# Optimization experiments

Hardware: AMD Instinct MI355X
Metric: run time of the kernel (lower is better)

## Reference

```python
import jax, jax.numpy as jnp
import numpy as np

FP4_MAX = 6.0  # largest E2M1 magnitude


def _round_fp4(y):
    # Round to nearest value on the FP4 E2M1 grid {0, +-0.5, 1, 1.5, 2, 3, 4, 6}.
    a = jnp.abs(y)
    e = jnp.floor(jnp.log2(jnp.maximum(a, 1.0)))  # 0 for a<2, 1 for [2,4), 2 for >=4
    step = jnp.exp2(e - 1.0)                      # grid spacing: 0.5, 1, 2
    q = jnp.clip(jnp.round(a / step) * step, 0.0, FP4_MAX)
    return jnp.sign(y) * q


def _ste_round_fp4(y):
    # straight-through estimator: identity gradient through the rounding
    return y + jax.lax.stop_gradient(_round_fp4(y) - y)


def _mxfp4_quant(x, group_size, eps=None):
    # Groupwise MXFP4 quant-dequant along the last axis.
    lead, d = x.shape[:-1], x.shape[-1]
    g = d // group_size
    xg = x.reshape(lead + (g, group_size))
    amax = jnp.max(jnp.abs(xg), axis=-1, keepdims=True)
    # shared exponent per MX spec: floor(log2(amax)) - emax_elem (emax_elem = 2 for FP4)
    exps = jnp.where(amax > 0.0,
                     jnp.floor(jnp.log2(jnp.maximum(amax, 1e-30))) - 2.0,
                     0.0)
    scale = jnp.exp2(exps)
    if eps is not None:
        # learnable (adversarially perturbed) per-group scale epsilon
        scale = scale * (1.0 + eps[..., None])
    y = xg / scale
    xq = _ste_round_fp4(y) * scale
    return xq.reshape(x.shape), jnp.squeeze(exps, -1)


def setup_inputs() -> dict:
    key = jax.random.key(0)
    ks = jax.random.split(key, 4)
    B, S, DIN, DOUT, GS = 4, 2048, 4096, 4096, 32
    x = jax.random.normal(ks[0], (B, S, DIN), jnp.float32)
    weight_fp = jax.random.normal(ks[1], (DOUT, DIN), jnp.float32) * 0.02  # frozen FP weight
    bias = jax.random.normal(ks[2], (DOUT,), jnp.float32) * 0.01
    eps = jnp.zeros((DOUT, DIN // GS), jnp.float32)  # learnable weight-quant epsilon
    adversarial_delta = jax.random.normal(ks[3], (DOUT, DIN // GS), jnp.float32) * 0.01
    return {"x": x, "adversarial_delta": adversarial_delta,
            "weight_fp": weight_fp, "bias": bias, "eps": eps}


def reference(x, adversarial_delta, weight_fp, bias, eps):
    GS = 32
    # dynamic activation MXFP4 quantization
    x_q, act_exps = _mxfp4_quant(x, GS)
    # weight MXFP4 quantization with learnable + adversarial epsilon
    eps_eff = eps + adversarial_delta
    w_q, w_exps = _mxfp4_quant(weight_fp, GS, eps_eff)
    # F.linear(x_q, w_q, bias)
    out = jnp.einsum('bsi,oi->bso', x_q, w_q) + bias
    return (out, eps_eff, w_exps, act_exps)
```

## Files before the change

kernel.cpp:

```cpp
#include <hip/hip_runtime.h>
#include <hip/hip_bf16.h>

#define DIN   4096
#define DOUT  4096
#define MROWS 8192
#define GSIZE 32
#define NGPR  (DIN / GSIZE)
#define NG_ACT (MROWS * NGPR)
#define NG_W   (DOUT * NGPR)

typedef __bf16 bf16_t;
typedef __attribute__((ext_vector_type(8))) __bf16 bf16x8;
typedef __attribute__((ext_vector_type(4))) float f32x4;

typedef const __attribute__((address_space(1))) void* gptr_t;
typedef __attribute__((address_space(3))) void* lptr_t;

__device__ __forceinline__ float fp4_round(float y) {
  float a  = __builtin_fabsf(y);
  float am = fmaxf(a, 1.0f);
  int   e  = (int)((__float_as_uint(am) >> 23) & 255u) - 127;
  float step = __uint_as_float((unsigned)(e - 1 + 127) << 23);
  float q = rintf(a / step) * step;
  q = fminf(q, 6.0f);
  return copysignf(q, y);
}

__global__ __launch_bounds__(256) void act_quant(const float* __restrict__ x,
                                                 bf16_t* __restrict__ xq,
                                                 float* __restrict__ exps_out) {
  int g = blockIdx.x * 256 + threadIdx.x;
  const float4* xp = reinterpret_cast<const float4*>(x) + (size_t)g * 8;
  float v[32];
  float amax = 0.f;
#pragma unroll
  for (int i = 0; i < 8; ++i) {
    float4 t = xp[i];
    v[4*i+0] = t.x; v[4*i+1] = t.y; v[4*i+2] = t.z; v[4*i+3] = t.w;
    amax = fmaxf(amax, fmaxf(fmaxf(__builtin_fabsf(t.x), __builtin_fabsf(t.y)),
                             fmaxf(__builtin_fabsf(t.z), __builtin_fabsf(t.w))));
  }
  float exps = 0.f;
  if (amax > 0.f) {
    float am = fmaxf(amax, 1e-30f);
    exps = (float)((int)((__float_as_uint(am) >> 23) & 255u) - 129);
  }
  float scale = __uint_as_float((unsigned)((int)exps + 127) << 23);
  float inv   = __uint_as_float((unsigned)(127 - (int)exps) << 23);
  bf16x8 hv[4];
#pragma unroll
  for (int i = 0; i < 32; ++i) {
    float q = fp4_round(v[i] * inv) * scale;
    hv[i >> 3][i & 7] = (bf16_t)q;
  }
  bf16x8* dst = reinterpret_cast<bf16x8*>(xq + (size_t)g * 32);
#pragma unroll
  for (int i = 0; i < 4; ++i) dst[i] = hv[i];
  exps_out[g] = exps;
}

__global__ __launch_bounds__(256) void w_quant(const float* __restrict__ w,
                                               const float* __restrict__ eps,
                                               const float* __restrict__ adv,
                                               bf16_t* __restrict__ wq,
                                               float* __restrict__ eps_eff_out,
                                               float* __restrict__ w_exps_out) {
  int g = blockIdx.x * 256 + threadIdx.x;
  float ee = eps[g] + adv[g];
  eps_eff_out[g] = ee;
  const float4* wp = reinterpret_cast<const float4*>(w) + (size_t)g * 8;
  float v[32];
  float amax = 0.f;
#pragma unroll
  for (int i = 0; i < 8; ++i) {
    float4 t = wp[i];
    v[4*i+0] = t.x; v[4*i+1] = t.y; v[4*i+2] = t.z; v[4*i+3] = t.w;
    amax = fmaxf(amax, fmaxf(fmaxf(__builtin_fabsf(t.x), __builtin_fabsf(t.y)),
                             fmaxf(__builtin_fabsf(t.z), __builtin_fabsf(t.w))));
  }
  float exps = 0.f;
  if (amax > 0.f) {
    float am = fmaxf(amax, 1e-30f);
    exps = (float)((int)((__float_as_uint(am) >> 23) & 255u) - 129);
  }
  w_exps_out[g] = exps;
  float p2   = __uint_as_float((unsigned)((int)exps + 127) << 23);
  float scale = p2 * (1.0f + ee);
  bf16x8 hv[4];
#pragma unroll
  for (int i = 0; i < 32; ++i) {
    float q = fp4_round(v[i] / scale) * scale;
    hv[i >> 3][i & 7] = (bf16_t)q;
  }
  bf16x8* dst = reinterpret_cast<bf16x8*>(wq + (size_t)g * 32);
#pragma unroll
  for (int i = 0; i < 4; ++i) dst[i] = hv[i];
}

#define BK 32
__global__ __launch_bounds__(256) void gemm_bt(const bf16_t* __restrict__ A,
                                               const bf16_t* __restrict__ B,
                                               const float* __restrict__ bias,
                                               float* __restrict__ C) {
  __shared__ bf16_t As[128 * BK];
  __shared__ bf16_t Bs[128 * BK];
  const int tid  = threadIdx.x;
  const int wave = tid >> 6;
  const int lane = tid & 63;
  const int tm0  = blockIdx.y * 128;
  const int tn0  = blockIdx.x * 128;
  const int wr   = wave >> 1;
  const int wc   = wave & 1;

  const int lrow = lane >> 2;
  const int lcol = (lane & 3) * 8;

  f32x4 acc[4][4] = {};

  const int afrag_off = (wr * 64 + (lane & 15)) * BK + (lane >> 4) * 8;
  const int bfrag_off = (wc * 64 + (lane & 15)) * BK + (lane >> 4) * 8;

  for (int kt = 0; kt < DIN / BK; ++kt) {
#pragma unroll
    for (int i = 0; i < 2; ++i) {
      const int r0 = wave * 32 + i * 16;
      const bf16_t* ga = A + (size_t)(tm0 + r0 + lrow) * DIN + kt * BK + lcol;
      __builtin_amdgcn_global_load_lds((gptr_t)ga, (lptr_t)(As + r0 * BK), 16, 0, 0);
      const bf16_t* gb = B + (size_t)(tn0 + r0 + lrow) * DIN + kt * BK + lcol;
      __builtin_amdgcn_global_load_lds((gptr_t)gb, (lptr_t)(Bs + r0 * BK), 16, 0, 0);
    }
    asm volatile("s_waitcnt vmcnt(0)" ::: "memory");
    __syncthreads();

    bf16x8 af[4], bfr[4];
#pragma unroll
    for (int t = 0; t < 4; ++t) {
      af[t]  = *reinterpret_cast<const bf16x8*>(&As[t * 16 * BK + afrag_off]);
      bfr[t] = *reinterpret_cast<const bf16x8*>(&Bs[t * 16 * BK + bfrag_off]);
    }
#pragma unroll
    for (int am = 0; am < 4; ++am)
#pragma unroll
      for (int bn = 0; bn < 4; ++bn)
        acc[am][bn] = __builtin_amdgcn_mfma_f32_16x16x32_bf16(af[am], bfr[bn], acc[am][bn], 0, 0, 0);
    __syncthreads();
  }

  const int row_base = tm0 + wr * 64 + ((lane >> 4) << 2);
  const int col_base = tn0 + wc * 64 + (lane & 15);
#pragma unroll
  for (int bn = 0; bn < 4; ++bn) {
    float bv = bias[col_base + bn * 16];
#pragma unroll
    for (int am = 0; am < 4; ++am) {
#pragma unroll
      for (int j = 0; j < 4; ++j) {
        C[(size_t)(row_base + am * 16 + j) * DOUT + col_base + bn * 16] = acc[am][bn][j] + bv;
      }
    }
  }
}

extern "C" void kernel_launch(void* const* d_in, const int* in_sizes, int n_in,
                              void* d_out, int out_size, void* d_ws, size_t ws_size,
                              hipStream_t stream) {
  const float* x    = (const float*)d_in[0];
  const float* adv  = (const float*)d_in[1];
  const float* wfp  = (const float*)d_in[2];
  const float* bias = (const float*)d_in[3];
  const float* eps  = (const float*)d_in[4];

  float* out      = (float*)d_out;
  float* eps_eff  = out + (size_t)MROWS * DOUT;
  float* w_exps   = eps_eff + NG_W;
  float* act_exps = w_exps + NG_W;

  bf16_t* xq = (bf16_t*)d_ws;
  bf16_t* wq = (bf16_t*)d_ws + (size_t)MROWS * DIN;

  act_quant<<<NG_ACT / 256, 256, 0, stream>>>(x, xq, act_exps);
  w_quant<<<NG_W / 256, 256, 0, stream>>>(wfp, eps, adv, wq, eps_eff, w_exps);
  gemm_bt<<<dim3(DOUT / 128, MROWS / 128), 256, 0, stream>>>(xq, wq, bias, out);
}
```

Measured before the change: 373.2 us.

## Rewrite GEMM with 256x256 tiles, double-buffered LDS, swizzle and XCD-aware block mapping

Replaces the 128x128 single-buffered bf16 GEMM with a 512-thread 256x256-tile kernel using BK=64. Global-to-LDS loads for the next k-tile are issued before computing the current one, so memory transfer overlaps compute. It also adds an XOR swizzle on LDS slots to avoid bank conflicts, a block-index remap that groups tiles per XCD, and setprio around the MFMA bursts. The larger per-wave accumulator (8x4 tiles) raises register pressure and limits occupancy to one block per CU.

After: 451.5 us. 21.0% more time.

```diff
diff --git a/kernel.cpp b/kernel.cpp
--- a/kernel.cpp
+++ b/kernel.cpp
@@ -97,68 +97,102 @@
   for (int i = 0; i < 4; ++i) dst[i] = hv[i];
 }
 
-#define BK 32
-__global__ __launch_bounds__(256) void gemm_bt(const bf16_t* __restrict__ A,
-                                               const bf16_t* __restrict__ B,
-                                               const float* __restrict__ bias,
-                                               float* __restrict__ C) {
-  __shared__ bf16_t As[128 * BK];
-  __shared__ bf16_t Bs[128 * BK];
+#define TILE_BYTES 32768
+
+__global__ __launch_bounds__(512, 1) void gemm_bt(const bf16_t* __restrict__ A,
+                                                  const bf16_t* __restrict__ B,
+                                                  const float* __restrict__ bias,
+                                                  float* __restrict__ C) {
+  __shared__ bf16_t sA[2 * TILE_BYTES / 2];
+  __shared__ bf16_t sB[2 * TILE_BYTES / 2];
   const int tid  = threadIdx.x;
   const int wave = tid >> 6;
   const int lane = tid & 63;
-  const int tm0  = blockIdx.y * 128;
-  const int tn0  = blockIdx.x * 128;
-  const int wr   = wave >> 1;
-  const int wc   = wave & 1;
-
-  const int lrow = lane >> 2;
-  const int lcol = (lane & 3) * 8;
-
-  f32x4 acc[4][4] = {};
-
-  const int afrag_off = (wr * 64 + (lane & 15)) * BK + (lane >> 4) * 8;
-  const int bfrag_off = (wc * 64 + (lane & 15)) * BK + (lane >> 4) * 8;
-
-  for (int kt = 0; kt < DIN / BK; ++kt) {
-#pragma unroll
-    for (int i = 0; i < 2; ++i) {
-      const int r0 = wave * 32 + i * 16;
-      const bf16_t* ga = A + (size_t)(tm0 + r0 + lrow) * DIN + kt * BK + lcol;
-      __builtin_amdgcn_global_load_lds((gptr_t)ga, (lptr_t)(As + r0 * BK), 16, 0, 0);
-      const bf16_t* gb = B + (size_t)(tn0 + r0 + lrow) * DIN + kt * BK + lcol;
-      __builtin_amdgcn_global_load_lds((gptr_t)gb, (lptr_t)(Bs + r0 * BK), 16, 0, 0);
+
+  const int swz = (blockIdx.x & 7) * 64 + (blockIdx.x >> 3);
+  const int tm0 = (swz >> 4) * 256;
+  const int tn0 = (swz & 15) * 256;
+
+  const int wr = wave >> 2;
+  const int wc = wave & 3;
+
+  const int slog = ((lane & 7) ^ (lane >> 3)) * 8;
+  const bf16_t* ag = A + (size_t)(tm0 + wave * 32 + (lane >> 3)) * DIN + slog;
+  const bf16_t* bg = B + (size_t)(tn0 + wave * 32 + (lane >> 3)) * DIN + slog;
+  const int lds_woff = wave * 32 * 64;
+
+#define STAGE(d, kt) do {                                                          \
+    const bf16_t* ap_ = ag + (kt) * 64;                                            \
+    const bf16_t* bp_ = bg + (kt) * 64;                                            \
+    _Pragma("unroll")                                                              \
+    for (int i_ = 0; i_ < 4; ++i_) {                                               \
+      __builtin_amdgcn_global_load_lds((gptr_t)(ap_ + (size_t)i_ * 8 * DIN),       \
+          (lptr_t)(sA + (d) * (TILE_BYTES/2) + lds_woff + i_ * 512), 16, 0, 0);    \
+      __builtin_amdgcn_global_load_lds((gptr_t)(bp_ + (size_t)i_ * 8 * DIN),       \
+          (lptr_t)(sB + (d) * (TILE_BYTES/2) + lds_woff + i_ * 512), 16, 0, 0);    \
+    }                                                                              \
+  } while (0)
+
+  const int arow_b = (wr * 128 + (lane & 15)) * 128;
+  const int brow_b = (wc * 64  + (lane & 15)) * 128;
+  const int slot0  = (((lane >> 4) ^ (lane & 7)) << 4);
+
+  f32x4 acc[8][4] = {};
+
+  STAGE(0, 0);
+  const int NT = DIN / 64;
+  for (int j = 0; j < NT; ++j) {
+    const int cur = j & 1;
+    if (j + 1 < NT) {
+      STAGE(cur ^ 1, j + 1);
+      asm volatile("s_waitcnt vmcnt(8)" ::: "memory");
+    } else {
+      asm volatile("s_waitcnt vmcnt(0)" ::: "memory");
     }
-    asm volatile("s_waitcnt vmcnt(0)" ::: "memory");
-    __syncthreads();
-
-    bf16x8 af[4], bfr[4];
-#pragma unroll
-    for (int t = 0; t < 4; ++t) {
-      af[t]  = *reinterpret_cast<const bf16x8*>(&As[t * 16 * BK + afrag_off]);
-      bfr[t] = *reinterpret_cast<const bf16x8*>(&Bs[t * 16 * BK + bfrag_off]);
+    asm volatile("s_barrier" ::: "memory");
+
+    const char* bufA = (const char*)sA + cur * TILE_BYTES;
+    const char* bufB = (const char*)sB + cur * TILE_BYTES;
+#pragma unroll
+    for (int p = 0; p < 4; ++p) {
+      const int kk = p & 1;
+      const int nh = p >> 1;
+      const int so = slot0 ^ (kk << 6);
+      bf16x8 af[8], bq[2];
+#pragma unroll
+      for (int m = 0; m < 8; ++m)
+        af[m] = *reinterpret_cast<const bf16x8*>(bufA + arow_b + m * 2048 + so);
+#pragma unroll
+      for (int t = 0; t < 2; ++t)
+        bq[t] = *reinterpret_cast<const bf16x8*>(bufB + brow_b + (nh * 2 + t) * 2048 + so);
+
+      asm volatile("s_barrier" ::: "memory");
+      __builtin_amdgcn_s_setprio(1);
+#pragma unroll
+      for (int t = 0; t < 2; ++t)
+#pragma unroll
+        for (int m = 0; m < 8; ++m)
+          acc[m][nh * 2 + t] =
+              __builtin_amdgcn_mfma_f32_16x16x32_bf16(af[m], bq[t], acc[m][nh * 2 + t], 0, 0, 0);
+      __builtin_amdgcn_s_setprio(0);
+      asm volatile("s_barrier" ::: "memory");
     }
-#pragma unroll
-    for (int am = 0; am < 4; ++am)
-#pragma unroll
-      for (int bn = 0; bn < 4; ++bn)
-        acc[am][bn] = __builtin_amdgcn_mfma_f32_16x16x32_bf16(af[am], bfr[bn], acc[am][bn], 0, 0, 0);
-    __syncthreads();
-  }
-
-  const int row_base = tm0 + wr * 64 + ((lane >> 4) << 2);
-  const int col_base = tn0 + wc * 64 + (lane & 15);
-#pragma unroll
-  for (int bn = 0; bn < 4; ++bn) {
-    float bv = bias[col_base + bn * 16];
-#pragma unroll
-    for (int am = 0; am < 4; ++am) {
-#pragma unroll
-      for (int j = 0; j < 4; ++j) {
-        C[(size_t)(row_base + am * 16 + j) * DOUT + col_base + bn * 16] = acc[am][bn][j] + bv;
+  }
+
+  const int r0 = tm0 + wr * 128 + ((lane >> 4) << 2);
+  const int c0 = tn0 + wc * 64 + (lane & 15);
+#pragma unroll
+  for (int n = 0; n < 4; ++n) {
+    float bv = bias[c0 + n * 16];
+#pragma unroll
+    for (int m = 0; m < 8; ++m) {
+#pragma unroll
+      for (int jj = 0; jj < 4; ++jj) {
+        C[(size_t)(r0 + m * 16 + jj) * DOUT + c0 + n * 16] = acc[m][n][jj] + bv;
       }
     }
   }
+#undef STAGE
 }
 
 extern "C" void kernel_launch(void* const* d_in, const int* in_sizes, int n_in,
@@ -180,5 +214,5 @@
 
   act_quant<<<NG_ACT / 256, 256, 0, stream>>>(x, xq, act_exps);
   w_quant<<<NG_W / 256, 256, 0, stream>>>(wfp, eps, adv, wq, eps_eff, w_exps);
-  gemm_bt<<<dim3(DOUT / 128, MROWS / 128), 256, 0, stream>>>(xq, wq, bias, out);
-}
+  gemm_bt<<<dim3((MROWS / 256) * (DOUT / 256)), 512, 0, stream>>>(xq, wq, bias, out);
+}
```

## Triple-buffer GEMM LDS staging with swizzled layout and XCD-aware block mapping

Applied to the files above, without the earlier changes.

Replaces the single-buffered GEMM main loop with a three-stage LDS ring, so global-to-LDS loads for tiles k+1 and k+2 are in flight while tile k is consumed, using vmcnt-based waits and one barrier per iteration. Adds an XOR swizzle on the LDS column slot to cut bank conflicts on fragment reads. Uses a 1D grid with block-index remapping so that blocks landing on the same XCD share row and column tiles, and sets launch_bounds occupancy to 3. The cost is more shared memory per block and more hand-ordered synchronization, which is fragile if the wait counts are wrong.

Result: slower. 406.0 us (+8.8%).

```diff
diff --git a/kernel.cpp b/kernel.cpp
--- a/kernel.cpp
+++ b/kernel.cpp
@@ -97,68 +97,94 @@
   for (int i = 0; i < 4; ++i) dst[i] = hv[i];
 }
 
-#define BK 32
-__global__ __launch_bounds__(256) void gemm_bt(const bf16_t* __restrict__ A,
-                                               const bf16_t* __restrict__ B,
-                                               const float* __restrict__ bias,
-                                               float* __restrict__ C) {
-  __shared__ bf16_t As[128 * BK];
-  __shared__ bf16_t Bs[128 * BK];
+__global__ __launch_bounds__(256, 3) void gemm_bt(const bf16_t* __restrict__ A,
+                                                  const bf16_t* __restrict__ B,
+                                                  const float* __restrict__ bias,
+                                                  float* __restrict__ C) {
+  __shared__ bf16_t sA[3 * 4096];
+  __shared__ bf16_t sB[3 * 4096];
   const int tid  = threadIdx.x;
   const int wave = tid >> 6;
   const int lane = tid & 63;
-  const int tm0  = blockIdx.y * 128;
-  const int tn0  = blockIdx.x * 128;
-  const int wr   = wave >> 1;
-  const int wc   = wave & 1;
-
-  const int lrow = lane >> 2;
-  const int lcol = (lane & 3) * 8;
+
+  const int swz = (blockIdx.x & 7) * 256 + (blockIdx.x >> 3);
+  const int tm0 = (swz >> 5) * 128;
+  const int tn0 = (swz & 31) * 128;
+
+  const int wr = wave >> 1;
+  const int wc = wave & 1;
+
+  const int lr = lane >> 2;
+  const int lc = ((lane & 3) ^ ((lane >> 4) & 3)) * 8;
+  const bf16_t* gA = A + (size_t)(tm0 + wave * 32 + lr) * DIN + lc;
+  const bf16_t* gB = B + (size_t)(tn0 + wave * 32 + lr) * DIN + lc;
+  const int dst0 = wave * 1024;
+
+#define STG(kt, bf) do {                                                            \
+    const bf16_t* a_ = gA + (size_t)(kt) * 32;                                      \
+    const bf16_t* b_ = gB + (size_t)(kt) * 32;                                      \
+    __builtin_amdgcn_global_load_lds((gptr_t)a_,                                    \
+        (lptr_t)(sA + (bf) * 4096 + dst0), 16, 0, 0);                               \
+    __builtin_amdgcn_global_load_lds((gptr_t)(a_ + (size_t)16 * DIN),               \
+        (lptr_t)(sA + (bf) * 4096 + dst0 + 512), 16, 0, 0);                         \
+    __builtin_amdgcn_global_load_lds((gptr_t)b_,                                    \
+        (lptr_t)(sB + (bf) * 4096 + dst0), 16, 0, 0);                               \
+    __builtin_amdgcn_global_load_lds((gptr_t)(b_ + (size_t)16 * DIN),               \
+        (lptr_t)(sB + (bf) * 4096 + dst0 + 512), 16, 0, 0);                         \
+  } while (0)
+
+  const int slot  = (((lane >> 4) ^ ((lane >> 2) & 3)) << 4);
+  const int apart = (wr * 64 + (lane & 15)) * 64 + slot;
+  const int bpart = (wc * 64 + (lane & 15)) * 64 + slot;
 
   f32x4 acc[4][4] = {};
 
-  const int afrag_off = (wr * 64 + (lane & 15)) * BK + (lane >> 4) * 8;
-  const int bfrag_off = (wc * 64 + (lane & 15)) * BK + (lane >> 4) * 8;
-
-  for (int kt = 0; kt < DIN / BK; ++kt) {
-#pragma unroll
-    for (int i = 0; i < 2; ++i) {
-      const int r0 = wave * 32 + i * 16;
-      const bf16_t* ga = A + (size_t)(tm0 + r0 + lrow) * DIN + kt * BK + lcol;
-      __builtin_amdgcn_global_load_lds((gptr_t)ga, (lptr_t)(As + r0 * BK), 16, 0, 0);
-      const bf16_t* gb = B + (size_t)(tn0 + r0 + lrow) * DIN + kt * BK + lcol;
-      __builtin_amdgcn_global_load_lds((gptr_t)gb, (lptr_t)(Bs + r0 * BK), 16, 0, 0);
+  STG(0, 0); STG(1, 1);
+  asm volatile("s_waitcnt vmcnt(4)");
+  __builtin_amdgcn_s_barrier();
+  __builtin_amdgcn_sched_barrier(0);
+
+  for (int j = 0; j < 128; ++j) {
+    if (j + 2 < 128) STG(j + 2, (j + 2) % 3);
+    const char* bA = (const char*)sA + (j % 3) * 8192;
+    const char* bB = (const char*)sB + (j % 3) * 8192;
+    bf16x8 a[4], b[4];
+#pragma unroll
+    for (int m = 0; m < 4; ++m)
+      a[m] = *reinterpret_cast<const bf16x8*>(bA + apart + m * 1024);
+#pragma unroll
+    for (int n = 0; n < 4; ++n)
+      b[n] = *reinterpret_cast<const bf16x8*>(bB + bpart + n * 1024);
+#pragma unroll
+    for (int m = 0; m < 4; ++m)
+#pragma unroll
+      for (int n = 0; n < 4; ++n)
+        acc[m][n] = __builtin_amdgcn_mfma_f32_16x16x32_bf16(a[m], b[n], acc[m][n], 0, 0, 0);
+    __builtin_amdgcn_sched_barrier(0);
+    asm volatile("s_waitcnt lgkmcnt(0)");
+    if (j < 126) {
+      asm volatile("s_waitcnt vmcnt(4)");
+    } else {
+      asm volatile("s_waitcnt vmcnt(0)");
     }
-    asm volatile("s_waitcnt vmcnt(0)" ::: "memory");
-    __syncthreads();
-
-    bf16x8 af[4], bfr[4];
-#pragma unroll
-    for (int t = 0; t < 4; ++t) {
-      af[t]  = *reinterpret_cast<const bf16x8*>(&As[t * 16 * BK + afrag_off]);
-      bfr[t] = *reinterpret_cast<const bf16x8*>(&Bs[t * 16 * BK + bfrag_off]);
-    }
-#pragma unroll
-    for (int am = 0; am < 4; ++am)
-#pragma unroll
-      for (int bn = 0; bn < 4; ++bn)
-        acc[am][bn] = __builtin_amdgcn_mfma_f32_16x16x32_bf16(af[am], bfr[bn], acc[am][bn], 0, 0, 0);
-    __syncthreads();
-  }
-
-  const int row_base = tm0 + wr * 64 + ((lane >> 4) << 2);
-  const int col_base = tn0 + wc * 64 + (lane & 15);
-#pragma unroll
-  for (int bn = 0; bn < 4; ++bn) {
-    float bv = bias[col_base + bn * 16];
-#pragma unroll
-    for (int am = 0; am < 4; ++am) {
-#pragma unroll
-      for (int j = 0; j < 4; ++j) {
-        C[(size_t)(row_base + am * 16 + j) * DOUT + col_base + bn * 16] = acc[am][bn][j] + bv;
+    __builtin_amdgcn_s_barrier();
+    __builtin_amdgcn_sched_barrier(0);
+  }
+
+  const int r0 = tm0 + wr * 64 + ((lane >> 4) << 2);
+  const int c0 = tn0 + wc * 64 + (lane & 15);
+#pragma unroll
+  for (int n = 0; n < 4; ++n) {
+    float bv = bias[c0 + n * 16];
+#pragma unroll
+    for (int m = 0; m < 4; ++m) {
+#pragma unroll
+      for (int jj = 0; jj < 4; ++jj) {
+        C[(size_t)(r0 + m * 16 + jj) * DOUT + c0 + n * 16] = acc[m][n][jj] + bv;
       }
     }
   }
+#undef STG
 }
 
 extern "C" void kernel_launch(void* const* d_in, const int* in_sizes, int n_in,
@@ -180,5 +206,5 @@
 
   act_quant<<<NG_ACT / 256, 256, 0, stream>>>(x, xq, act_exps);
   w_quant<<<NG_W / 256, 256, 0, stream>>>(wfp, eps, adv, wq, eps_eff, w_exps);
-  gemm_bt<<<dim3(DOUT / 128, MROWS / 128), 256, 0, stream>>>(xq, wq, bias, out);
-}
+  gemm_bt<<<dim3((MROWS / 128) * (DOUT / 128)), 256, 0, stream>>>(xq, wq, bias, out);
+}
```
